# Kernel tuning notes

Measured on AMD Instinct MI355X. Metric: run time of the kernel, lower is better.

## Reference

```python
import jax, jax.numpy as jnp
import numpy as np

B, N, DIM, H, DH = 2, 2048, 512, 8, 64
EPS = 1e-3  # eps added after relu feature map, per original


def setup_inputs() -> dict:
    key = jax.random.key(0)
    k0, k1, k2, k3, k4 = jax.random.split(key, 5)
    s_in = 1.0 / np.sqrt(DIM)
    s_out = 1.0 / np.sqrt(H * DH)
    return {
        "x": jax.random.normal(k0, (B, N, DIM), jnp.float32),
        "Wq": jax.random.normal(k1, (DIM, H * DH), jnp.float32) * s_in,
        "Wk": jax.random.normal(k2, (DIM, H * DH), jnp.float32) * s_in,
        "Wv": jax.random.normal(k3, (DIM, H * DH), jnp.float32) * s_in,
        "Wo": jax.random.normal(k4, (H * DH, DIM), jnp.float32) * s_out,
        "bo": jnp.zeros((DIM,), jnp.float32),
    }


def causal_linear_attn(q, k, v, eps=EPS):
    # bucket_size == 1 path of the original causal_linear_attn (blindspot_size=1):
    # relu feature map + eps, running cumsums of k and of the outer product k v^T.
    q = jax.nn.relu(q) + eps
    k = jax.nn.relu(k) + eps
    k_cum = jnp.cumsum(k, axis=2)                                  # [b,h,n,d]
    ctx = jnp.cumsum(k[..., :, None] * v[..., None, :], axis=2)    # [b,h,n,d,e]
    d_inv = 1.0 / jnp.einsum('bhnd,bhnd->bhn', q, k_cum)           # [b,h,n]
    return jnp.einsum('bhnd,bhnde,bhn->bhne', q, ctx, d_inv)       # [b,h,n,e]


def reference(x, Wq, Wk, Wv, Wo, bo):
    b, n, _ = x.shape
    split = lambda t: t.reshape(b, n, H, DH).transpose(0, 2, 1, 3)  # [b,h,n,dh]
    q = split(x @ Wq)
    k = split(x @ Wk)
    v = split(x @ Wv)
    out = causal_linear_attn(q, k, v)
    out = out.transpose(0, 2, 1, 3).reshape(b, n, H * DH)
    return out @ Wo + bo
```

## Files before the change

### kernel.cpp

```cpp
#include <hip/hip_runtime.h>

constexpr int kB   = 2;
constexpr int kN   = 2048;
constexpr int kDIM = 512;
constexpr int kH   = 8;
constexpr int kDH  = 64;
constexpr int kBH  = kB * kH;
constexpr int NROWS = kB * kN;
constexpr int CHUNK = 64;
constexpr int NCH   = kN / CHUNK;
constexpr int CBSTRIDE = kDH * kDH + kDH;
constexpr float kEPS = 1e-3f;

typedef _Float16 f16x8 __attribute__((ext_vector_type(8)));
typedef _Float16 f16x4 __attribute__((ext_vector_type(4)));
typedef float    floatx4 __attribute__((ext_vector_type(4)));

__device__ __forceinline__ void async_copy16(void* lds, const void* g) {
    __builtin_amdgcn_global_load_lds(
        (const __attribute__((address_space(1))) void*)g,
        (__attribute__((address_space(3))) void*)lds,
        16, 0, 0);
}

__global__ __launch_bounds__(256)
void convert_x_kernel(const float* __restrict__ x, _Float16* __restrict__ xh)
{
    const int i = blockIdx.x * 256 + threadIdx.x;
    const float4 a = *(const float4*)(x + (size_t)i * 8);
    const float4 b = *(const float4*)(x + (size_t)i * 8 + 4);
    f16x8 o;
    o[0] = (_Float16)a.x; o[1] = (_Float16)a.y; o[2] = (_Float16)a.z; o[3] = (_Float16)a.w;
    o[4] = (_Float16)b.x; o[5] = (_Float16)b.y; o[6] = (_Float16)b.z; o[7] = (_Float16)b.w;
    *(f16x8*)(xh + (size_t)i * 8) = o;
}

__global__ __launch_bounds__(256)
void convert_wT_kernel(const float* __restrict__ Wq, const float* __restrict__ Wk,
                       const float* __restrict__ Wv, const float* __restrict__ Wo,
                       _Float16* __restrict__ WT, _Float16* __restrict__ WoT)
{
    __shared__ float tile[32][33];
    const int z = blockIdx.z;
    const float* src = (z == 0) ? Wq : (z == 1) ? Wk : (z == 2) ? Wv : Wo;
    _Float16* dst = (z < 3) ? (WT + (size_t)z * 512 * 512) : WoT;
    const int r0 = blockIdx.y * 32, c0 = blockIdx.x * 32;
    const int tr = threadIdx.x >> 5, tc = threadIdx.x & 31;
    #pragma unroll
    for (int i = 0; i < 4; ++i)
        tile[tr + 8 * i][tc] = src[(size_t)(r0 + tr + 8 * i) * 512 + c0 + tc];
    __syncthreads();
    #pragma unroll
    for (int i = 0; i < 4; ++i)
        dst[(size_t)(c0 + tr + 8 * i) * 512 + r0 + tc] = (_Float16)tile[tc][tr + 8 * i];
}

template<int MODE>
__global__ __launch_bounds__(256)
void mfma_gemm_kernel(const _Float16* __restrict__ A,
                      const _Float16* __restrict__ BT,
                      const float* __restrict__ bo,
                      float* __restrict__ outf,
                      _Float16* __restrict__ qh,
                      _Float16* __restrict__ khb,
                      _Float16* __restrict__ kTh,
                      _Float16* __restrict__ vTh)
{
    constexpr int BM = 128, BN = 128, BK = 64, K = 512;
    __shared__ _Float16 As[BM * BK];
    __shared__ _Float16 Bs[BN * BK];

    const int t = threadIdx.x;
    const int l = t & 63;
    const int w = t >> 6;
    const int wm = w >> 1, wn = w & 1;
    const int m0 = blockIdx.x * BM;
    const int n0 = blockIdx.y * BN;

    const int r15 = l & 15, kq = l >> 4, sw = r15 & 7;

    floatx4 acc[4][4];
    #pragma unroll
    for (int mi = 0; mi < 4; ++mi)
        #pragma unroll
        for (int ni = 0; ni < 4; ++ni)
            acc[mi][ni] = (floatx4){0.f, 0.f, 0.f, 0.f};

    const int srow  = t >> 3;
    const int sslot = t & 7;

    const char* Abase = (const char*)(A + (size_t)m0 * K);
    const char* Bbase = (const char*)(BT + (size_t)n0 * K);
    char* AsB = (char*)As;
    char* BsB = (char*)Bs;

    const char* ArdB = (const char*)As + (wm * 64 + r15) * 128;
    const char* BrdB = (const char*)Bs + (wn * 64 + r15) * 128;
    const int sw0 = ((kq ^ sw) << 4);
    const int sw1 = (((4 + kq) ^ sw) << 4);

    for (int k0 = 0; k0 < K; k0 += BK) {
        #pragma unroll
        for (int i = 0; i < 4; ++i) {
            const int row = i * 32 + srow;
            const int gsl = sslot ^ (row & 7);
            async_copy16(AsB + row * 128 + sslot * 16,
                         Abase + (size_t)row * (K * 2) + k0 * 2 + gsl * 16);
            async_copy16(BsB + row * 128 + sslot * 16,
                         Bbase + (size_t)row * (K * 2) + k0 * 2 + gsl * 16);
        }
        __syncthreads();

        f16x8 af[4][2], bf[4][2];
        #pragma unroll
        for (int i = 0; i < 4; ++i) {
            af[i][0] = *(const f16x8*)(ArdB + i * 2048 + sw0);
            af[i][1] = *(const f16x8*)(ArdB + i * 2048 + sw1);
            bf[i][0] = *(const f16x8*)(BrdB + i * 2048 + sw0);
            bf[i][1] = *(const f16x8*)(BrdB + i * 2048 + sw1);
        }
        #pragma unroll
        for (int kk = 0; kk < 2; ++kk)
            #pragma unroll
            for (int mi = 0; mi < 4; ++mi)
                #pragma unroll
                for (int ni = 0; ni < 4; ++ni)
                    acc[mi][ni] = __builtin_amdgcn_mfma_f32_16x16x32_f16(
                        af[mi][kk], bf[ni][kk], acc[mi][ni], 0, 0, 0);
        __syncthreads();
    }

    if (MODE == 0) {
        #pragma unroll
        for (int ni = 0; ni < 4; ++ni) {
            const int col = n0 + wn * 64 + ni * 16 + r15;
            const int which = col >> 9;
            const int h = (col >> 6) & 7, e = col & 63;
            #pragma unroll
            for (int mi = 0; mi < 4; ++mi) {
                const int row0 = m0 + wm * 64 + mi * 16 + kq * 4;
                const int b = row0 >> 11, nn = row0 & 2047;
                const int bh = b * 8 + h;
                float vv[4];
                #pragma unroll
                for (int r = 0; r < 4; ++r) {
                    float v = acc[mi][ni][r];
                    if (which < 2) v = fmaxf(v, 0.f) + kEPS;
                    vv[r] = v;
                }
                if (which == 0) {
                    #pragma unroll
                    for (int r = 0; r < 4; ++r)
                        qh[((size_t)bh * kN + nn + r) * 64 + e] = (_Float16)vv[r];
                } else if (which == 1) {
                    #pragma unroll
                    for (int r = 0; r < 4; ++r)
                        khb[((size_t)bh * kN + nn + r) * 64 + e] = (_Float16)vv[r];
                    f16x4 t4;
                    t4[0] = (_Float16)vv[0]; t4[1] = (_Float16)vv[1];
                    t4[2] = (_Float16)vv[2]; t4[3] = (_Float16)vv[3];
                    *(f16x4*)(kTh + ((size_t)bh * 64 + e) * kN + nn) = t4;
                } else {
                    f16x4 t4;
                    t4[0] = (_Float16)vv[0]; t4[1] = (_Float16)vv[1];
                    t4[2] = (_Float16)vv[2]; t4[3] = (_Float16)vv[3];
                    *(f16x4*)(vTh + ((size_t)bh * 64 + e) * kN + nn) = t4;
                }
            }
        }
    } else {
        #pragma unroll
        for (int ni = 0; ni < 4; ++ni) {
            const int col = n0 + wn * 64 + ni * 16 + r15;
            const float bias = bo[col];
            #pragma unroll
            for (int mi = 0; mi < 4; ++mi) {
                const int row = m0 + wm * 64 + mi * 16 + kq * 4;
                #pragma unroll
                for (int r = 0; r < 4; ++r)
                    outf[(size_t)(row + r) * 512 + col] = acc[mi][ni][r] + bias;
            }
        }
    }
}

__global__ __launch_bounds__(256)
void chunk_sum_kernel(const _Float16* __restrict__ kTh, const _Float16* __restrict__ vTh,
                      float* __restrict__ cbuf)
{
    const int ch = blockIdx.x, bh = blockIdx.y;
    const int t = threadIdx.x, l = t & 63, w = t >> 6;
    const int r15 = l & 15, kq = l >> 4;

    const _Float16* vbase = vTh + (size_t)bh * 64 * kN + ch * 64;
    const _Float16* kbase = kTh + (size_t)bh * 64 * kN + ch * 64;

    f16x8 av[2], bk[4][2];
    #pragma unroll
    for (int kk = 0; kk < 2; ++kk) {
        av[kk] = *(const f16x8*)(vbase + (size_t)(w * 16 + r15) * kN + kk * 32 + kq * 8);
        #pragma unroll
        for (int ni = 0; ni < 4; ++ni)
            bk[ni][kk] = *(const f16x8*)(kbase + (size_t)(ni * 16 + r15) * kN + kk * 32 + kq * 8);
    }
    floatx4 acc[4];
    #pragma unroll
    for (int ni = 0; ni < 4; ++ni) acc[ni] = (floatx4){0.f, 0.f, 0.f, 0.f};
    #pragma unroll
    for (int kk = 0; kk < 2; ++kk)
        #pragma unroll
        for (int ni = 0; ni < 4; ++ni)
            acc[ni] = __builtin_amdgcn_mfma_f32_16x16x32_f16(av[kk], bk[ni][kk], acc[ni], 0, 0, 0);

    float* out = cbuf + ((size_t)bh * NCH + ch) * CBSTRIDE;
    #pragma unroll
    for (int ni = 0; ni < 4; ++ni)
        #pragma unroll
        for (int r = 0; r < 4; ++r)
            out[(size_t)(w * 16 + kq * 4 + r) * 64 + ni * 16 + r15] = acc[ni][r];

    if (t < 64) {
        const _Float16* kp = kbase + (size_t)t * kN;
        float z = 0.f;
        #pragma unroll
        for (int j = 0; j < 8; ++j) {
            f16x8 v8 = *(const f16x8*)(kp + j * 8);
            #pragma unroll
            for (int u = 0; u < 8; ++u) z += (float)v8[u];
        }
        out[4096 + t] = z;
    }
}

__global__ __launch_bounds__(256)
void prefix_kernel(const float* __restrict__ cbuf, _Float16* __restrict__ spre16,
                   float* __restrict__ zpre)
{
    const int bh = blockIdx.y;
    const int i = blockIdx.x * 256 + threadIdx.x;
    if (i >= CBSTRIDE) return;
    const float* src = cbuf + (size_t)bh * NCH * CBSTRIDE + i;
    _Float16* dst = spre16 + (size_t)bh * NCH * CBSTRIDE + i;
    float* zp = zpre + (size_t)bh * NCH * 64;
    const bool isz = (i >= 4096);
    float vals[NCH];
    #pragma unroll
    for (int c = 0; c < NCH; ++c) vals[c] = src[(size_t)c * CBSTRIDE];
    float a = 0.f;
    #pragma unroll
    for (int c = 0; c < NCH; ++c) {
        dst[(size_t)c * CBSTRIDE] = (_Float16)a;
        if (isz) zp[c * 64 + (i - 4096)] = a;
        a += vals[c];
    }
}

__global__ __launch_bounds__(256)
void chunk_out_kernel(const _Float16* __restrict__ qh, const _Float16* __restrict__ khb,
                      const _Float16* __restrict__ vTh, const _Float16* __restrict__ spre16,
                      const float* __restrict__ zpre, _Float16* __restrict__ attnh)
{
    const int ch = blockIdx.x, bh = blockIdx.y;
    const int t = threadIdx.x, l = t & 63, w = t >> 6;
    const int r15 = l & 15, kq = l >> 4;

    __shared__ _Float16 Plds[64 * 64];
    __shared__ float denp[64];
    __shared__ float denf[64];

    const size_t rowbase = (size_t)bh * kN + ch * 64;

    f16x8 aq[2], bk[4][2];
    #pragma unroll
    for (int kk = 0; kk < 2; ++kk) {
        aq[kk] = *(const f16x8*)(qh + (rowbase + w * 16 + r15) * 64 + kk * 32 + kq * 8);
        #pragma unroll
        for (int ni = 0; ni < 4; ++ni)
            bk[ni][kk] = *(const f16x8*)(khb + (rowbase + ni * 16 + r15) * 64 + kk * 32 + kq * 8);
    }
    floatx4 sacc[4];
    #pragma unroll
    for (int ni = 0; ni < 4; ++ni) sacc[ni] = (floatx4){0.f, 0.f, 0.f, 0.f};
    #pragma unroll
    for (int kk = 0; kk < 2; ++kk)
        #pragma unroll
        for (int ni = 0; ni < 4; ++ni)
            sacc[ni] = __builtin_amdgcn_mfma_f32_16x16x32_f16(aq[kk], bk[ni][kk], sacc[ni], 0, 0, 0);

    const int qrow = w * 16 + kq * 4;
    float psum[4] = {0.f, 0.f, 0.f, 0.f};
    #pragma unroll
    for (int ni = 0; ni < 4; ++ni) {
        const int m = ni * 16 + r15;
        #pragma unroll
        for (int r = 0; r < 4; ++r) {
            const int row = qrow + r;
            const float v = (m <= row) ? sacc[ni][r] : 0.f;
            psum[r] += v;
            const int byte = row * 128 + ((((unsigned)m >> 3) ^ (row & 7)) << 4) + (m & 7) * 2;
            *(_Float16*)((char*)Plds + byte) = (_Float16)v;
        }
    }
    #pragma unroll
    for (int r = 0; r < 4; ++r) {
        float p = psum[r];
        p += __shfl_xor(p, 1, 16);
        p += __shfl_xor(p, 2, 16);
        p += __shfl_xor(p, 4, 16);
        p += __shfl_xor(p, 8, 16);
        if (r15 == 0) denp[qrow + r] = p;
    }
    __syncthreads();

    if (t < 64) {
        const _Float16* qp = qh + (rowbase + t) * 64;
        const float* zp = zpre + ((size_t)bh * NCH + ch) * 64;
        float s = denp[t];
        #pragma unroll
        for (int j = 0; j < 8; ++j) {
            f16x8 q8 = *(const f16x8*)(qp + j * 8);
            #pragma unroll
            for (int u = 0; u < 8; ++u) s += (float)q8[u] * zp[j * 8 + u];
        }
        denf[t] = 1.0f / s;
    }

    f16x8 ap[2], bv[4][2], bs[4][2];
    #pragma unroll
    for (int km = 0; km < 2; ++km)
        ap[km] = *(const f16x8*)((char*)Plds + (w * 16 + r15) * 128 +
                                 (((km * 4 + kq) ^ (r15 & 7)) << 4));
    #pragma unroll
    for (int ni = 0; ni < 4; ++ni) {
        #pragma unroll
        for (int km = 0; km < 2; ++km)
            bv[ni][km] = *(const f16x8*)(vTh + ((size_t)bh * 64 + ni * 16 + r15) * kN +
                                         ch * 64 + km * 32 + kq * 8);
    }
    const _Float16* sp = spre16 + ((size_t)bh * NCH + ch) * CBSTRIDE;
    #pragma unroll
    for (int ni = 0; ni < 4; ++ni)
        #pragma unroll
        for (int kd = 0; kd < 2; ++kd)
            bs[ni][kd] = *(const f16x8*)(sp + (size_t)(ni * 16 + r15) * 64 + kd * 32 + kq * 8);

    floatx4 oacc[4];
    #pragma unroll
    for (int ni = 0; ni < 4; ++ni) oacc[ni] = (floatx4){0.f, 0.f, 0.f, 0.f};
    #pragma unroll
    for (int km = 0; km < 2; ++km)
        #pragma unroll
        for (int ni = 0; ni < 4; ++ni)
            oacc[ni] = __builtin_amdgcn_mfma_f32_16x16x32_f16(ap[km], bv[ni][km], oacc[ni], 0, 0, 0);
    #pragma unroll
    for (int kd = 0; kd < 2; ++kd)
        #pragma unroll
        for (int ni = 0; ni < 4; ++ni)
            oacc[ni] = __builtin_amdgcn_mfma_f32_16x16x32_f16(aq[kd], bs[ni][kd], oacc[ni], 0, 0, 0);
    __syncthreads();

    const int b = bh >> 3, h = bh & 7;
    #pragma unroll
    for (int ni = 0; ni < 4; ++ni) {
        const int e = ni * 16 + r15;
        #pragma unroll
        for (int r = 0; r < 4; ++r) {
            const int qn = qrow + r;
            const float ov = oacc[ni][r] * denf[qn];
            attnh[((size_t)(b * kN + ch * 64 + qn)) * 512 + h * 64 + e] = (_Float16)ov;
        }
    }
}

extern "C" void kernel_launch(void* const* d_in, const int* in_sizes, int n_in,
                              void* d_out, int out_size, void* d_ws, size_t ws_size,
                              hipStream_t stream)
{
    const float* x  = (const float*)d_in[0];
    const float* Wq = (const float*)d_in[1];
    const float* Wk = (const float*)d_in[2];
    const float* Wv = (const float*)d_in[3];
    const float* Wo = (const float*)d_in[4];
    const float* bo = (const float*)d_in[5];
    float* out = (float*)d_out;

    char* ws = (char*)d_ws;
    _Float16* qh     = (_Float16*)(ws + 0);
    _Float16* khb    = (_Float16*)(ws + 4194304);
    _Float16* kTh    = (_Float16*)(ws + 8388608);
    _Float16* vTh    = (_Float16*)(ws + 12582912);
    float*    cbuf   = (float*)(ws + 16777216);
    _Float16* spre16 = (_Float16*)(ws + 25296896);
    float*    zpre   = (float*)(ws + 29556736);
    _Float16* xh     = (_Float16*)(ws + 29687808);
    _Float16* WT     = (_Float16*)(ws + 33882112);
    _Float16* WoT    = (_Float16*)(ws + 35454976);
    _Float16* attnh  = xh;

    convert_x_kernel<<<1024, 256, 0, stream>>>(x, xh);
    convert_wT_kernel<<<dim3(16, 16, 4), 256, 0, stream>>>(Wq, Wk, Wv, Wo, WT, WoT);
    mfma_gemm_kernel<0><<<dim3(NROWS / 128, 12), 256, 0, stream>>>(
        xh, WT, nullptr, nullptr, qh, khb, kTh, vTh);
    chunk_sum_kernel<<<dim3(NCH, kBH), 256, 0, stream>>>(kTh, vTh, cbuf);
    prefix_kernel<<<dim3(17, kBH), 256, 0, stream>>>(cbuf, spre16, zpre);
    chunk_out_kernel<<<dim3(NCH, kBH), 256, 0, stream>>>(qh, khb, vTh, spre16, zpre, attnh);
    mfma_gemm_kernel<1><<<dim3(NROWS / 128, 4), 256, 0, stream>>>(
        attnh, WoT, bo, out, nullptr, nullptr, nullptr, nullptr);
}
```

Baseline: 56.48 us.

## Fuse attention stages with grid barriers and convert x inside QKV GEMM

Merges the chunk-sum, prefix-scan and chunk-output kernels into one persistent kernel that synchronises the whole grid with atomic-counter barriers. The fp32-to-fp16 conversion of x moves into the QKV GEMM's A-tile load, which removes the separate convert kernel and its round trip through memory. The grid is transposed so consecutive blocks share an A row tile. This cuts four launches in exchange for spin-wait barriers, which deadlock unless all 512 blocks are co-resident, and it replaces the async A loads with synchronous converting loads.

```diff
diff --git a/kernel.cpp b/kernel.cpp
--- a/kernel.cpp
+++ b/kernel.cpp
@@ -23,23 +23,26 @@
         16, 0, 0);
 }
 
+__device__ __forceinline__ void grid_barrier(unsigned* cnt, unsigned target) {
+    __syncthreads();
+    if (threadIdx.x == 0) {
+        __threadfence();
+        __hip_atomic_fetch_add(cnt, 1u, __ATOMIC_ACQ_REL, __HIP_MEMORY_SCOPE_AGENT);
+        while (__hip_atomic_load(cnt, __ATOMIC_ACQUIRE, __HIP_MEMORY_SCOPE_AGENT) < target)
+            __builtin_amdgcn_s_sleep(2);
+        __threadfence();
+    }
+    __syncthreads();
+}
+
 __global__ __launch_bounds__(256)
-void convert_x_kernel(const float* __restrict__ x, _Float16* __restrict__ xh)
+void prep_kernel(const float* __restrict__ Wq, const float* __restrict__ Wk,
+                 const float* __restrict__ Wv, const float* __restrict__ Wo,
+                 _Float16* __restrict__ WT, _Float16* __restrict__ WoT,
+                 unsigned* __restrict__ cnt)
 {
-    const int i = blockIdx.x * 256 + threadIdx.x;
-    const float4 a = *(const float4*)(x + (size_t)i * 8);
-    const float4 b = *(const float4*)(x + (size_t)i * 8 + 4);
-    f16x8 o;
-    o[0] = (_Float16)a.x; o[1] = (_Float16)a.y; o[2] = (_Float16)a.z; o[3] = (_Float16)a.w;
-    o[4] = (_Float16)b.x; o[5] = (_Float16)b.y; o[6] = (_Float16)b.z; o[7] = (_Float16)b.w;
-    *(f16x8*)(xh + (size_t)i * 8) = o;
-}
-
-__global__ __launch_bounds__(256)
-void convert_wT_kernel(const float* __restrict__ Wq, const float* __restrict__ Wk,
-                       const float* __restrict__ Wv, const float* __restrict__ Wo,
-                       _Float16* __restrict__ WT, _Float16* __restrict__ WoT)
-{
+    if (blockIdx.x == 0 && blockIdx.y == 0 && blockIdx.z == 0 && threadIdx.x < 4)
+        cnt[threadIdx.x] = 0u;
     __shared__ float tile[32][33];
     const int z = blockIdx.z;
     const float* src = (z == 0) ? Wq : (z == 1) ? Wk : (z == 2) ? Wv : Wo;
@@ -57,7 +60,8 @@
 
 template<int MODE>
 __global__ __launch_bounds__(256)
-void mfma_gemm_kernel(const _Float16* __restrict__ A,
+void mfma_gemm_kernel(const float* __restrict__ Af32,
+                      const _Float16* __restrict__ Af16,
                       const _Float16* __restrict__ BT,
                       const float* __restrict__ bo,
                       float* __restrict__ outf,
@@ -66,16 +70,16 @@
                       _Float16* __restrict__ kTh,
                       _Float16* __restrict__ vTh)
 {
-    constexpr int BM = 128, BN = 128, BK = 64, K = 512;
-    __shared__ _Float16 As[BM * BK];
-    __shared__ _Float16 Bs[BN * BK];
+    constexpr int K = 512;
+    __shared__ _Float16 As[128 * 64];
+    __shared__ _Float16 Bs[128 * 64];
 
     const int t = threadIdx.x;
     const int l = t & 63;
     const int w = t >> 6;
     const int wm = w >> 1, wn = w & 1;
-    const int m0 = blockIdx.x * BM;
-    const int n0 = blockIdx.y * BN;
+    const int m0 = blockIdx.y * 128;
+    const int n0 = blockIdx.x * 128;
 
     const int r15 = l & 15, kq = l >> 4, sw = r15 & 7;
 
@@ -89,7 +93,6 @@
     const int srow  = t >> 3;
     const int sslot = t & 7;
 
-    const char* Abase = (const char*)(A + (size_t)m0 * K);
     const char* Bbase = (const char*)(BT + (size_t)n0 * K);
     char* AsB = (char*)As;
     char* BsB = (char*)Bs;
@@ -99,15 +102,38 @@
     const int sw0 = ((kq ^ sw) << 4);
     const int sw1 = (((4 + kq) ^ sw) << 4);
 
-    for (int k0 = 0; k0 < K; k0 += BK) {
+    for (int k0 = 0; k0 < K; k0 += 64) {
         #pragma unroll
         for (int i = 0; i < 4; ++i) {
             const int row = i * 32 + srow;
             const int gsl = sslot ^ (row & 7);
-            async_copy16(AsB + row * 128 + sslot * 16,
-                         Abase + (size_t)row * (K * 2) + k0 * 2 + gsl * 16);
             async_copy16(BsB + row * 128 + sslot * 16,
                          Bbase + (size_t)row * (K * 2) + k0 * 2 + gsl * 16);
+        }
+        if (MODE == 0) {
+            #pragma unroll
+            for (int i = 0; i < 4; ++i) {
+                const int s = i * 256 + t;
+                const int row = s >> 3, sl = s & 7;
+                const float* xp = Af32 + (size_t)(m0 + row) * K + k0 + sl * 8;
+                const float4 a0 = *(const float4*)(xp);
+                const float4 a1 = *(const float4*)(xp + 4);
+                f16x8 v;
+                v[0] = (_Float16)a0.x; v[1] = (_Float16)a0.y;
+                v[2] = (_Float16)a0.z; v[3] = (_Float16)a0.w;
+                v[4] = (_Float16)a1.x; v[5] = (_Float16)a1.y;
+                v[6] = (_Float16)a1.z; v[7] = (_Float16)a1.w;
+                *(f16x8*)(AsB + row * 128 + ((sl ^ (row & 7)) << 4)) = v;
+            }
+        } else {
+            const char* Abase = (const char*)(Af16 + (size_t)m0 * K);
+            #pragma unroll
+            for (int i = 0; i < 4; ++i) {
+                const int row = i * 32 + srow;
+                const int gsl = sslot ^ (row & 7);
+                async_copy16(AsB + row * 128 + sslot * 16,
+                             Abase + (size_t)row * (K * 2) + k0 * 2 + gsl * 16);
+            }
         }
         __syncthreads();
 
@@ -185,88 +211,87 @@
 }
 
 __global__ __launch_bounds__(256)
-void chunk_sum_kernel(const _Float16* __restrict__ kTh, const _Float16* __restrict__ vTh,
-                      float* __restrict__ cbuf)
+void mid_kernel(const _Float16* __restrict__ qh, const _Float16* __restrict__ khb,
+                const _Float16* __restrict__ kTh, const _Float16* __restrict__ vTh,
+                float* __restrict__ cbuf, _Float16* __restrict__ spre16,
+                float* __restrict__ zpre, _Float16* __restrict__ attnh,
+                unsigned* __restrict__ cnt)
 {
     const int ch = blockIdx.x, bh = blockIdx.y;
     const int t = threadIdx.x, l = t & 63, w = t >> 6;
     const int r15 = l & 15, kq = l >> 4;
 
-    const _Float16* vbase = vTh + (size_t)bh * 64 * kN + ch * 64;
-    const _Float16* kbase = kTh + (size_t)bh * 64 * kN + ch * 64;
-
-    f16x8 av[2], bk[4][2];
-    #pragma unroll
-    for (int kk = 0; kk < 2; ++kk) {
-        av[kk] = *(const f16x8*)(vbase + (size_t)(w * 16 + r15) * kN + kk * 32 + kq * 8);
-        #pragma unroll
-        for (int ni = 0; ni < 4; ++ni)
-            bk[ni][kk] = *(const f16x8*)(kbase + (size_t)(ni * 16 + r15) * kN + kk * 32 + kq * 8);
-    }
-    floatx4 acc[4];
-    #pragma unroll
-    for (int ni = 0; ni < 4; ++ni) acc[ni] = (floatx4){0.f, 0.f, 0.f, 0.f};
-    #pragma unroll
-    for (int kk = 0; kk < 2; ++kk)
-        #pragma unroll
-        for (int ni = 0; ni < 4; ++ni)
-            acc[ni] = __builtin_amdgcn_mfma_f32_16x16x32_f16(av[kk], bk[ni][kk], acc[ni], 0, 0, 0);
-
-    float* out = cbuf + ((size_t)bh * NCH + ch) * CBSTRIDE;
-    #pragma unroll
-    for (int ni = 0; ni < 4; ++ni)
-        #pragma unroll
-        for (int r = 0; r < 4; ++r)
-            out[(size_t)(w * 16 + kq * 4 + r) * 64 + ni * 16 + r15] = acc[ni][r];
-
-    if (t < 64) {
-        const _Float16* kp = kbase + (size_t)t * kN;
-        float z = 0.f;
-        #pragma unroll
-        for (int j = 0; j < 8; ++j) {
-            f16x8 v8 = *(const f16x8*)(kp + j * 8);
-            #pragma unroll
-            for (int u = 0; u < 8; ++u) z += (float)v8[u];
-        }
-        out[4096 + t] = z;
-    }
-}
-
-__global__ __launch_bounds__(256)
-void prefix_kernel(const float* __restrict__ cbuf, _Float16* __restrict__ spre16,
-                   float* __restrict__ zpre)
-{
-    const int bh = blockIdx.y;
-    const int i = blockIdx.x * 256 + threadIdx.x;
-    if (i >= CBSTRIDE) return;
-    const float* src = cbuf + (size_t)bh * NCH * CBSTRIDE + i;
-    _Float16* dst = spre16 + (size_t)bh * NCH * CBSTRIDE + i;
-    float* zp = zpre + (size_t)bh * NCH * 64;
-    const bool isz = (i >= 4096);
-    float vals[NCH];
-    #pragma unroll
-    for (int c = 0; c < NCH; ++c) vals[c] = src[(size_t)c * CBSTRIDE];
-    float a = 0.f;
-    #pragma unroll
-    for (int c = 0; c < NCH; ++c) {
-        dst[(size_t)c * CBSTRIDE] = (_Float16)a;
-        if (isz) zp[c * 64 + (i - 4096)] = a;
-        a += vals[c];
-    }
-}
-
-__global__ __launch_bounds__(256)
-void chunk_out_kernel(const _Float16* __restrict__ qh, const _Float16* __restrict__ khb,
-                      const _Float16* __restrict__ vTh, const _Float16* __restrict__ spre16,
-                      const float* __restrict__ zpre, _Float16* __restrict__ attnh)
-{
-    const int ch = blockIdx.x, bh = blockIdx.y;
-    const int t = threadIdx.x, l = t & 63, w = t >> 6;
-    const int r15 = l & 15, kq = l >> 4;
-
     __shared__ _Float16 Plds[64 * 64];
     __shared__ float denp[64];
     __shared__ float denf[64];
+
+    {
+        const _Float16* vbase = vTh + (size_t)bh * 64 * kN + ch * 64;
+        const _Float16* kbase = kTh + (size_t)bh * 64 * kN + ch * 64;
+        f16x8 av[2], bk[4][2];
+        #pragma unroll
+        for (int kk = 0; kk < 2; ++kk) {
+            av[kk] = *(const f16x8*)(vbase + (size_t)(w * 16 + r15) * kN + kk * 32 + kq * 8);
+            #pragma unroll
+            for (int ni = 0; ni < 4; ++ni)
+                bk[ni][kk] = *(const f16x8*)(kbase + (size_t)(ni * 16 + r15) * kN + kk * 32 + kq * 8);
+        }
+        floatx4 sa[4];
+        #pragma unroll
+        for (int ni = 0; ni < 4; ++ni) sa[ni] = (floatx4){0.f, 0.f, 0.f, 0.f};
+        #pragma unroll
+        for (int kk = 0; kk < 2; ++kk)
+            #pragma unroll
+            for (int ni = 0; ni < 4; ++ni)
+                sa[ni] = __builtin_amdgcn_mfma_f32_16x16x32_f16(av[kk], bk[ni][kk], sa[ni], 0, 0, 0);
+
+        float* outp = cbuf + ((size_t)bh * NCH + ch) * CBSTRIDE;
+        #pragma unroll
+        for (int ni = 0; ni < 4; ++ni)
+            #pragma unroll
+            for (int r = 0; r < 4; ++r)
+                outp[(size_t)(w * 16 + kq * 4 + r) * 64 + ni * 16 + r15] = sa[ni][r];
+
+        if (t < 64) {
+            const _Float16* kp = kbase + (size_t)t * kN;
+            float z = 0.f;
+            #pragma unroll
+            for (int j = 0; j < 8; ++j) {
+                f16x8 v8 = *(const f16x8*)(kp + j * 8);
+                #pragma unroll
+                for (int u = 0; u < 8; ++u) z += (float)v8[u];
+            }
+            outp[4096 + t] = z;
+        }
+    }
+    grid_barrier(cnt, NCH * kBH);
+
+    {
+        const int col = ch * 130 + t;
+        if (t < 130) {
+            const float* src = cbuf + (size_t)bh * NCH * CBSTRIDE + col;
+            float vals[NCH];
+            #pragma unroll
+            for (int c = 0; c < NCH; ++c) vals[c] = src[(size_t)c * CBSTRIDE];
+            float a = 0.f;
+            if (col < 4096) {
+                _Float16* dst = spre16 + (size_t)bh * NCH * CBSTRIDE + col;
+                #pragma unroll
+                for (int c = 0; c < NCH; ++c) {
+                    dst[(size_t)c * CBSTRIDE] = (_Float16)a;
+                    a += vals[c];
+                }
+            } else {
+                float* zp = zpre + (size_t)bh * NCH * 64 + (col - 4096);
+                #pragma unroll
+                for (int c = 0; c < NCH; ++c) {
+                    zp[c * 64] = a;
+                    a += vals[c];
+                }
+            }
+        }
+    }
+    grid_barrier(cnt, 2 * NCH * kBH);
 
     const size_t rowbase = (size_t)bh * kN + ch * 64;
 
@@ -392,18 +417,16 @@
     float*    cbuf   = (float*)(ws + 16777216);
     _Float16* spre16 = (_Float16*)(ws + 25296896);
     float*    zpre   = (float*)(ws + 29556736);
-    _Float16* xh     = (_Float16*)(ws + 29687808);
+    _Float16* attnh  = (_Float16*)(ws + 29687808);
     _Float16* WT     = (_Float16*)(ws + 33882112);
     _Float16* WoT    = (_Float16*)(ws + 35454976);
-    _Float16* attnh  = xh;
-
-    convert_x_kernel<<<1024, 256, 0, stream>>>(x, xh);
-    convert_wT_kernel<<<dim3(16, 16, 4), 256, 0, stream>>>(Wq, Wk, Wv, Wo, WT, WoT);
-    mfma_gemm_kernel<0><<<dim3(NROWS / 128, 12), 256, 0, stream>>>(
-        xh, WT, nullptr, nullptr, qh, khb, kTh, vTh);
-    chunk_sum_kernel<<<dim3(NCH, kBH), 256, 0, stream>>>(kTh, vTh, cbuf);
-    prefix_kernel<<<dim3(17, kBH), 256, 0, stream>>>(cbuf, spre16, zpre);
-    chunk_out_kernel<<<dim3(NCH, kBH), 256, 0, stream>>>(qh, khb, vTh, spre16, zpre, attnh);
-    mfma_gemm_kernel<1><<<dim3(NROWS / 128, 4), 256, 0, stream>>>(
-        attnh, WoT, bo, out, nullptr, nullptr, nullptr, nullptr);
-}
+    unsigned* cnt    = (unsigned*)(ws + 35979264);
+
+    prep_kernel<<<dim3(16, 16, 4), 256, 0, stream>>>(Wq, Wk, Wv, Wo, WT, WoT, cnt);
+    mfma_gemm_kernel<0><<<dim3(12, NROWS / 128), 256, 0, stream>>>(
+        x, nullptr, WT, nullptr, nullptr, qh, khb, kTh, vTh);
+    mid_kernel<<<dim3(NCH, kBH), 256, 0, stream>>>(
+        qh, khb, kTh, vTh, cbuf, spre16, zpre, attnh, cnt);
+    mfma_gemm_kernel<1><<<dim3(4, NROWS / 128), 256, 0, stream>>>(
+        nullptr, attnh, WoT, bo, out, nullptr, nullptr, nullptr, nullptr);
+}
```

Measured after the change: 175.9 us. +211.5%, slower.

## Fuse x conversion into QKV GEMM and fuse output projection into chunk kernel

Applied to the files above, without the earlier changes.

The QKV GEMM now loads fp32 x directly and converts it to fp16 while staging into LDS, which removes the separate convert kernel and its round trip through global memory. The chunk output kernel becomes a 512-thread block that covers all 8 heads of a 64-row chunk. It stages the normalized attention output in LDS and immediately runs the Wo projection plus bias, writing the final fp32 output. This removes two launches and the attnh buffer traffic. The cost is fewer, larger blocks (64 in the epilogue) with WoT fragments read straight from global memory, and the A operand in the QKV GEMM is now loaded synchronously.

```diff
diff --git a/kernel.cpp b/kernel.cpp
--- a/kernel.cpp
+++ b/kernel.cpp
@@ -24,21 +24,9 @@
 }
 
 __global__ __launch_bounds__(256)
-void convert_x_kernel(const float* __restrict__ x, _Float16* __restrict__ xh)
-{
-    const int i = blockIdx.x * 256 + threadIdx.x;
-    const float4 a = *(const float4*)(x + (size_t)i * 8);
-    const float4 b = *(const float4*)(x + (size_t)i * 8 + 4);
-    f16x8 o;
-    o[0] = (_Float16)a.x; o[1] = (_Float16)a.y; o[2] = (_Float16)a.z; o[3] = (_Float16)a.w;
-    o[4] = (_Float16)b.x; o[5] = (_Float16)b.y; o[6] = (_Float16)b.z; o[7] = (_Float16)b.w;
-    *(f16x8*)(xh + (size_t)i * 8) = o;
-}
-
-__global__ __launch_bounds__(256)
-void convert_wT_kernel(const float* __restrict__ Wq, const float* __restrict__ Wk,
-                       const float* __restrict__ Wv, const float* __restrict__ Wo,
-                       _Float16* __restrict__ WT, _Float16* __restrict__ WoT)
+void prep_kernel(const float* __restrict__ Wq, const float* __restrict__ Wk,
+                 const float* __restrict__ Wv, const float* __restrict__ Wo,
+                 _Float16* __restrict__ WT, _Float16* __restrict__ WoT)
 {
     __shared__ float tile[32][33];
     const int z = blockIdx.z;
@@ -55,27 +43,24 @@
         dst[(size_t)(c0 + tr + 8 * i) * 512 + r0 + tc] = (_Float16)tile[tc][tr + 8 * i];
 }
 
-template<int MODE>
 __global__ __launch_bounds__(256)
-void mfma_gemm_kernel(const _Float16* __restrict__ A,
-                      const _Float16* __restrict__ BT,
-                      const float* __restrict__ bo,
-                      float* __restrict__ outf,
-                      _Float16* __restrict__ qh,
-                      _Float16* __restrict__ khb,
-                      _Float16* __restrict__ kTh,
-                      _Float16* __restrict__ vTh)
-{
-    constexpr int BM = 128, BN = 128, BK = 64, K = 512;
-    __shared__ _Float16 As[BM * BK];
-    __shared__ _Float16 Bs[BN * BK];
+void qkv_gemm_kernel(const float* __restrict__ Af32,
+                     const _Float16* __restrict__ BT,
+                     _Float16* __restrict__ qh,
+                     _Float16* __restrict__ khb,
+                     _Float16* __restrict__ kTh,
+                     _Float16* __restrict__ vTh)
+{
+    constexpr int K = 512;
+    __shared__ _Float16 As[128 * 64];
+    __shared__ _Float16 Bs[128 * 64];
 
     const int t = threadIdx.x;
     const int l = t & 63;
     const int w = t >> 6;
     const int wm = w >> 1, wn = w & 1;
-    const int m0 = blockIdx.x * BM;
-    const int n0 = blockIdx.y * BN;
+    const int m0 = blockIdx.y * 128;
+    const int n0 = blockIdx.x * 128;
 
     const int r15 = l & 15, kq = l >> 4, sw = r15 & 7;
 
@@ -89,7 +74,6 @@
     const int srow  = t >> 3;
     const int sslot = t & 7;
 
-    const char* Abase = (const char*)(A + (size_t)m0 * K);
     const char* Bbase = (const char*)(BT + (size_t)n0 * K);
     char* AsB = (char*)As;
     char* BsB = (char*)Bs;
@@ -99,15 +83,27 @@
     const int sw0 = ((kq ^ sw) << 4);
     const int sw1 = (((4 + kq) ^ sw) << 4);
 
-    for (int k0 = 0; k0 < K; k0 += BK) {
+    for (int k0 = 0; k0 < K; k0 += 64) {
         #pragma unroll
         for (int i = 0; i < 4; ++i) {
             const int row = i * 32 + srow;
             const int gsl = sslot ^ (row & 7);
-            async_copy16(AsB + row * 128 + sslot * 16,
-                         Abase + (size_t)row * (K * 2) + k0 * 2 + gsl * 16);
             async_copy16(BsB + row * 128 + sslot * 16,
                          Bbase + (size_t)row * (K * 2) + k0 * 2 + gsl * 16);
+        }
+        #pragma unroll
+        for (int i = 0; i < 4; ++i) {
+            const int s = i * 256 + t;
+            const int row = s >> 3, sl = s & 7;
+            const float* xp = Af32 + (size_t)(m0 + row) * K + k0 + sl * 8;
+            const float4 a0 = *(const float4*)(xp);
+            const float4 a1 = *(const float4*)(xp + 4);
+            f16x8 v;
+            v[0] = (_Float16)a0.x; v[1] = (_Float16)a0.y;
+            v[2] = (_Float16)a0.z; v[3] = (_Float16)a0.w;
+            v[4] = (_Float16)a1.x; v[5] = (_Float16)a1.y;
+            v[6] = (_Float16)a1.z; v[7] = (_Float16)a1.w;
+            *(f16x8*)(AsB + row * 128 + ((sl ^ (row & 7)) << 4)) = v;
         }
         __syncthreads();
 
@@ -130,55 +126,40 @@
         __syncthreads();
     }
 
-    if (MODE == 0) {
-        #pragma unroll
-        for (int ni = 0; ni < 4; ++ni) {
-            const int col = n0 + wn * 64 + ni * 16 + r15;
-            const int which = col >> 9;
-            const int h = (col >> 6) & 7, e = col & 63;
-            #pragma unroll
-            for (int mi = 0; mi < 4; ++mi) {
-                const int row0 = m0 + wm * 64 + mi * 16 + kq * 4;
-                const int b = row0 >> 11, nn = row0 & 2047;
-                const int bh = b * 8 + h;
-                float vv[4];
-                #pragma unroll
-                for (int r = 0; r < 4; ++r) {
-                    float v = acc[mi][ni][r];
-                    if (which < 2) v = fmaxf(v, 0.f) + kEPS;
-                    vv[r] = v;
-                }
-                if (which == 0) {
-                    #pragma unroll
-                    for (int r = 0; r < 4; ++r)
-                        qh[((size_t)bh * kN + nn + r) * 64 + e] = (_Float16)vv[r];
-                } else if (which == 1) {
-                    #pragma unroll
-                    for (int r = 0; r < 4; ++r)
-                        khb[((size_t)bh * kN + nn + r) * 64 + e] = (_Float16)vv[r];
-                    f16x4 t4;
-                    t4[0] = (_Float16)vv[0]; t4[1] = (_Float16)vv[1];
-                    t4[2] = (_Float16)vv[2]; t4[3] = (_Float16)vv[3];
-                    *(f16x4*)(kTh + ((size_t)bh * 64 + e) * kN + nn) = t4;
-                } else {
-                    f16x4 t4;
-                    t4[0] = (_Float16)vv[0]; t4[1] = (_Float16)vv[1];
-                    t4[2] = (_Float16)vv[2]; t4[3] = (_Float16)vv[3];
-                    *(f16x4*)(vTh + ((size_t)bh * 64 + e) * kN + nn) = t4;
-                }
+    #pragma unroll
+    for (int ni = 0; ni < 4; ++ni) {
+        const int col = n0 + wn * 64 + ni * 16 + r15;
+        const int which = col >> 9;
+        const int h = (col >> 6) & 7, e = col & 63;
+        #pragma unroll
+        for (int mi = 0; mi < 4; ++mi) {
+            const int row0 = m0 + wm * 64 + mi * 16 + kq * 4;
+            const int b = row0 >> 11, nn = row0 & 2047;
+            const int bh = b * 8 + h;
+            float vv[4];
+            #pragma unroll
+            for (int r = 0; r < 4; ++r) {
+                float v = acc[mi][ni][r];
+                if (which < 2) v = fmaxf(v, 0.f) + kEPS;
+                vv[r] = v;
             }
-        }
-    } else {
-        #pragma unroll
-        for (int ni = 0; ni < 4; ++ni) {
-            const int col = n0 + wn * 64 + ni * 16 + r15;
-            const float bias = bo[col];
-            #pragma unroll
-            for (int mi = 0; mi < 4; ++mi) {
-                const int row = m0 + wm * 64 + mi * 16 + kq * 4;
+            if (which == 0) {
                 #pragma unroll
                 for (int r = 0; r < 4; ++r)
-                    outf[(size_t)(row + r) * 512 + col] = acc[mi][ni][r] + bias;
+                    qh[((size_t)bh * kN + nn + r) * 64 + e] = (_Float16)vv[r];
+            } else if (which == 1) {
+                #pragma unroll
+                for (int r = 0; r < 4; ++r)
+                    khb[((size_t)bh * kN + nn + r) * 64 + e] = (_Float16)vv[r];
+                f16x4 t4;
+                t4[0] = (_Float16)vv[0]; t4[1] = (_Float16)vv[1];
+                t4[2] = (_Float16)vv[2]; t4[3] = (_Float16)vv[3];
+                *(f16x4*)(kTh + ((size_t)bh * 64 + e) * kN + nn) = t4;
+            } else {
+                f16x4 t4;
+                t4[0] = (_Float16)vv[0]; t4[1] = (_Float16)vv[1];
+                t4[2] = (_Float16)vv[2]; t4[3] = (_Float16)vv[3];
+                *(f16x4*)(vTh + ((size_t)bh * 64 + e) * kN + nn) = t4;
             }
         }
     }
@@ -255,88 +236,121 @@
     }
 }
 
-__global__ __launch_bounds__(256)
-void chunk_out_kernel(const _Float16* __restrict__ qh, const _Float16* __restrict__ khb,
-                      const _Float16* __restrict__ vTh, const _Float16* __restrict__ spre16,
-                      const float* __restrict__ zpre, _Float16* __restrict__ attnh)
-{
-    const int ch = blockIdx.x, bh = blockIdx.y;
-    const int t = threadIdx.x, l = t & 63, w = t >> 6;
+__global__ __launch_bounds__(512, 2)
+void chunk_epilogue_kernel(const _Float16* __restrict__ qh,
+                           const _Float16* __restrict__ khb,
+                           const _Float16* __restrict__ vTh,
+                           const _Float16* __restrict__ spre16,
+                           const float* __restrict__ zpre,
+                           const _Float16* __restrict__ WoT,
+                           const float* __restrict__ bo,
+                           float* __restrict__ outf)
+{
+    const int ch = blockIdx.x;
+    const int b  = blockIdx.y;
+    const int t = threadIdx.x;
+    const int w = t >> 6;
+    const int l = t & 63;
     const int r15 = l & 15, kq = l >> 4;
-
-    __shared__ _Float16 Plds[64 * 64];
-    __shared__ float denp[64];
-    __shared__ float denf[64];
-
-    const size_t rowbase = (size_t)bh * kN + ch * 64;
-
-    f16x8 aq[2], bk[4][2];
-    #pragma unroll
-    for (int kk = 0; kk < 2; ++kk) {
-        aq[kk] = *(const f16x8*)(qh + (rowbase + w * 16 + r15) * 64 + kk * 32 + kq * 8);
-        #pragma unroll
-        for (int ni = 0; ni < 4; ++ni)
-            bk[ni][kk] = *(const f16x8*)(khb + (rowbase + ni * 16 + r15) * 64 + kk * 32 + kq * 8);
-    }
-    floatx4 sacc[4];
-    #pragma unroll
-    for (int ni = 0; ni < 4; ++ni) sacc[ni] = (floatx4){0.f, 0.f, 0.f, 0.f};
-    #pragma unroll
-    for (int kk = 0; kk < 2; ++kk)
-        #pragma unroll
-        for (int ni = 0; ni < 4; ++ni)
-            sacc[ni] = __builtin_amdgcn_mfma_f32_16x16x32_f16(aq[kk], bk[ni][kk], sacc[ni], 0, 0, 0);
-
-    const int qrow = w * 16 + kq * 4;
-    float psum[4] = {0.f, 0.f, 0.f, 0.f};
-    #pragma unroll
-    for (int ni = 0; ni < 4; ++ni) {
-        const int m = ni * 16 + r15;
+    const int h = w;
+    const int bh = b * 8 + h;
+
+    __shared__ char smem[65536];
+    __shared__ float denp[8][64];
+    __shared__ float denf[8][64];
+
+    const size_t rowbase = (size_t)bh * kN + (size_t)ch * 64;
+
+    f16x8 aq[4][2];
+    #pragma unroll
+    for (int mi = 0; mi < 4; ++mi)
+        #pragma unroll
+        for (int kk = 0; kk < 2; ++kk)
+            aq[mi][kk] = *(const f16x8*)(qh + (rowbase + mi * 16 + r15) * 64 + kk * 32 + kq * 8);
+
+    floatx4 sacc[4][4];
+    #pragma unroll
+    for (int mi = 0; mi < 4; ++mi)
+        #pragma unroll
+        for (int ni = 0; ni < 4; ++ni)
+            sacc[mi][ni] = (floatx4){0.f, 0.f, 0.f, 0.f};
+    {
+        f16x8 bk[4][2];
+        #pragma unroll
+        for (int ni = 0; ni < 4; ++ni)
+            #pragma unroll
+            for (int kk = 0; kk < 2; ++kk)
+                bk[ni][kk] = *(const f16x8*)(khb + (rowbase + ni * 16 + r15) * 64 + kk * 32 + kq * 8);
+        #pragma unroll
+        for (int kk = 0; kk < 2; ++kk)
+            #pragma unroll
+            for (int mi = 0; mi < 4; ++mi)
+                #pragma unroll
+                for (int ni = 0; ni < 4; ++ni)
+                    sacc[mi][ni] = __builtin_amdgcn_mfma_f32_16x16x32_f16(
+                        aq[mi][kk], bk[ni][kk], sacc[mi][ni], 0, 0, 0);
+    }
+
+    char* P = smem + h * 8192;
+    float psum[4][4];
+    #pragma unroll
+    for (int mi = 0; mi < 4; ++mi)
+        #pragma unroll
+        for (int r = 0; r < 4; ++r) psum[mi][r] = 0.f;
+    #pragma unroll
+    for (int mi = 0; mi < 4; ++mi) {
+        #pragma unroll
+        for (int ni = 0; ni < 4; ++ni) {
+            const int m = ni * 16 + r15;
+            #pragma unroll
+            for (int r = 0; r < 4; ++r) {
+                const int row = mi * 16 + kq * 4 + r;
+                const float v = (m <= row) ? sacc[mi][ni][r] : 0.f;
+                psum[mi][r] += v;
+                const int byte = row * 128 + ((((unsigned)m >> 3) ^ (row & 7)) << 4) + (m & 7) * 2;
+                *(_Float16*)(P + byte) = (_Float16)v;
+            }
+        }
+    }
+    #pragma unroll
+    for (int mi = 0; mi < 4; ++mi) {
         #pragma unroll
         for (int r = 0; r < 4; ++r) {
-            const int row = qrow + r;
-            const float v = (m <= row) ? sacc[ni][r] : 0.f;
-            psum[r] += v;
-            const int byte = row * 128 + ((((unsigned)m >> 3) ^ (row & 7)) << 4) + (m & 7) * 2;
-            *(_Float16*)((char*)Plds + byte) = (_Float16)v;
-        }
-    }
-    #pragma unroll
-    for (int r = 0; r < 4; ++r) {
-        float p = psum[r];
-        p += __shfl_xor(p, 1, 16);
-        p += __shfl_xor(p, 2, 16);
-        p += __shfl_xor(p, 4, 16);
-        p += __shfl_xor(p, 8, 16);
-        if (r15 == 0) denp[qrow + r] = p;
-    }
-    __syncthreads();
-
-    if (t < 64) {
-        const _Float16* qp = qh + (rowbase + t) * 64;
+            float p = psum[mi][r];
+            p += __shfl_xor(p, 1, 16);
+            p += __shfl_xor(p, 2, 16);
+            p += __shfl_xor(p, 4, 16);
+            p += __shfl_xor(p, 8, 16);
+            if (r15 == 0) denp[h][mi * 16 + kq * 4 + r] = p;
+        }
+    }
+
+    {
+        const _Float16* qp = qh + (rowbase + l) * 64;
         const float* zp = zpre + ((size_t)bh * NCH + ch) * 64;
-        float s = denp[t];
+        float s = denp[h][l];
         #pragma unroll
         for (int j = 0; j < 8; ++j) {
             f16x8 q8 = *(const f16x8*)(qp + j * 8);
             #pragma unroll
             for (int u = 0; u < 8; ++u) s += (float)q8[u] * zp[j * 8 + u];
         }
-        denf[t] = 1.0f / s;
-    }
-
-    f16x8 ap[2], bv[4][2], bs[4][2];
-    #pragma unroll
-    for (int km = 0; km < 2; ++km)
-        ap[km] = *(const f16x8*)((char*)Plds + (w * 16 + r15) * 128 +
-                                 (((km * 4 + kq) ^ (r15 & 7)) << 4));
-    #pragma unroll
-    for (int ni = 0; ni < 4; ++ni) {
+        denf[h][l] = 1.0f / s;
+    }
+
+    f16x8 ap[4][2], bv[4][2], bs[4][2];
+    #pragma unroll
+    for (int mi = 0; mi < 4; ++mi)
+        #pragma unroll
+        for (int km = 0; km < 2; ++km)
+            ap[mi][km] = *(const f16x8*)(P + (mi * 16 + r15) * 128 +
+                                         (((km * 4 + kq) ^ (r15 & 7)) << 4));
+    #pragma unroll
+    for (int ni = 0; ni < 4; ++ni)
         #pragma unroll
         for (int km = 0; km < 2; ++km)
             bv[ni][km] = *(const f16x8*)(vTh + ((size_t)bh * 64 + ni * 16 + r15) * kN +
                                          ch * 64 + km * 32 + kq * 8);
-    }
     const _Float16* sp = spre16 + ((size_t)bh * NCH + ch) * CBSTRIDE;
     #pragma unroll
     for (int ni = 0; ni < 4; ++ni)
@@ -344,30 +358,85 @@
         for (int kd = 0; kd < 2; ++kd)
             bs[ni][kd] = *(const f16x8*)(sp + (size_t)(ni * 16 + r15) * 64 + kd * 32 + kq * 8);
 
-    floatx4 oacc[4];
-    #pragma unroll
-    for (int ni = 0; ni < 4; ++ni) oacc[ni] = (floatx4){0.f, 0.f, 0.f, 0.f};
+    floatx4 oacc[4][4];
+    #pragma unroll
+    for (int mi = 0; mi < 4; ++mi)
+        #pragma unroll
+        for (int ni = 0; ni < 4; ++ni)
+            oacc[mi][ni] = (floatx4){0.f, 0.f, 0.f, 0.f};
     #pragma unroll
     for (int km = 0; km < 2; ++km)
         #pragma unroll
-        for (int ni = 0; ni < 4; ++ni)
-            oacc[ni] = __builtin_amdgcn_mfma_f32_16x16x32_f16(ap[km], bv[ni][km], oacc[ni], 0, 0, 0);
+        for (int mi = 0; mi < 4; ++mi)
+            #pragma unroll
+            for (int ni = 0; ni < 4; ++ni)
+                oacc[mi][ni] = __builtin_amdgcn_mfma_f32_16x16x32_f16(
+                    ap[mi][km], bv[ni][km], oacc[mi][ni], 0, 0, 0);
     #pragma unroll
     for (int kd = 0; kd < 2; ++kd)
         #pragma unroll
-        for (int ni = 0; ni < 4; ++ni)
-            oacc[ni] = __builtin_amdgcn_mfma_f32_16x16x32_f16(aq[kd], bs[ni][kd], oacc[ni], 0, 0, 0);
+        for (int mi = 0; mi < 4; ++mi)
+            #pragma unroll
+            for (int ni = 0; ni < 4; ++ni)
+                oacc[mi][ni] = __builtin_amdgcn_mfma_f32_16x16x32_f16(
+                    aq[mi][kd], bs[ni][kd], oacc[mi][ni], 0, 0, 0);
+
     __syncthreads();
 
-    const int b = bh >> 3, h = bh & 7;
+    #pragma unroll
+    for (int mi = 0; mi < 4; ++mi) {
+        #pragma unroll
+        for (int ni = 0; ni < 4; ++ni) {
+            const int c = h * 64 + ni * 16 + r15;
+            const int slot = c >> 3;
+            #pragma unroll
+            for (int r = 0; r < 4; ++r) {
+                const int row = mi * 16 + kq * 4 + r;
+                const float ov = oacc[mi][ni][r] * denf[h][row];
+                const int byte = row * 1024 + ((slot ^ (row & 7)) << 4) + (c & 7) * 2;
+                *(_Float16*)(smem + byte) = (_Float16)ov;
+            }
+        }
+    }
+    __syncthreads();
+
+    floatx4 acc2[4][4];
+    #pragma unroll
+    for (int mi = 0; mi < 4; ++mi)
+        #pragma unroll
+        for (int ni = 0; ni < 4; ++ni)
+            acc2[mi][ni] = (floatx4){0.f, 0.f, 0.f, 0.f};
+
+    for (int kk = 0; kk < 16; ++kk) {
+        f16x8 af2[4], bf2[4];
+        #pragma unroll
+        for (int mi = 0; mi < 4; ++mi) {
+            const int row = mi * 16 + r15;
+            af2[mi] = *(const f16x8*)(smem + row * 1024 + (((kk * 4 + kq) ^ (row & 7)) << 4));
+        }
+        #pragma unroll
+        for (int ni = 0; ni < 4; ++ni)
+            bf2[ni] = *(const f16x8*)(WoT + ((size_t)(w * 64 + ni * 16 + r15)) * 512 +
+                                      kk * 32 + kq * 8);
+        #pragma unroll
+        for (int mi = 0; mi < 4; ++mi)
+            #pragma unroll
+            for (int ni = 0; ni < 4; ++ni)
+                acc2[mi][ni] = __builtin_amdgcn_mfma_f32_16x16x32_f16(
+                    af2[mi], bf2[ni], acc2[mi][ni], 0, 0, 0);
+    }
+
     #pragma unroll
     for (int ni = 0; ni < 4; ++ni) {
-        const int e = ni * 16 + r15;
-        #pragma unroll
-        for (int r = 0; r < 4; ++r) {
-            const int qn = qrow + r;
-            const float ov = oacc[ni][r] * denf[qn];
-            attnh[((size_t)(b * kN + ch * 64 + qn)) * 512 + h * 64 + e] = (_Float16)ov;
+        const int col = w * 64 + ni * 16 + r15;
+        const float bias = bo[col];
+        #pragma unroll
+        for (int mi = 0; mi < 4; ++mi) {
+            #pragma unroll
+            for (int r = 0; r < 4; ++r) {
+                const int rowg = b * 2048 + ch * 64 + mi * 16 + kq * 4 + r;
+                outf[(size_t)rowg * 512 + col] = acc2[mi][ni][r] + bias;
+            }
         }
     }
 }
@@ -392,18 +461,14 @@
     float*    cbuf   = (float*)(ws + 16777216);
     _Float16* spre16 = (_Float16*)(ws + 25296896);
     float*    zpre   = (float*)(ws + 29556736);
-    _Float16* xh     = (_Float16*)(ws + 29687808);
-    _Float16* WT     = (_Float16*)(ws + 33882112);
-    _Float16* WoT    = (_Float16*)(ws + 35454976);
-    _Float16* attnh  = xh;
-
-    convert_x_kernel<<<1024, 256, 0, stream>>>(x, xh);
-    convert_wT_kernel<<<dim3(16, 16, 4), 256, 0, stream>>>(Wq, Wk, Wv, Wo, WT, WoT);
-    mfma_gemm_kernel<0><<<dim3(NROWS / 128, 12), 256, 0, stream>>>(
-        xh, WT, nullptr, nullptr, qh, khb, kTh, vTh);
+    _Float16* WT     = (_Float16*)(ws + 29687808);
+    _Float16* WoT    = (_Float16*)(ws + 31260672);
+
+    prep_kernel<<<dim3(16, 16, 4), 256, 0, stream>>>(Wq, Wk, Wv, Wo, WT, WoT);
+    qkv_gemm_kernel<<<dim3(12, NROWS / 128), 256, 0, stream>>>(
+        x, WT, qh, khb, kTh, vTh);
     chunk_sum_kernel<<<dim3(NCH, kBH), 256, 0, stream>>>(kTh, vTh, cbuf);
     prefix_kernel<<<dim3(17, kBH), 256, 0, stream>>>(cbuf, spre16, zpre);
-    chunk_out_kernel<<<dim3(NCH, kBH), 256, 0, stream>>>(qh, khb, vTh, spre16, zpre, attnh);
-    mfma_gemm_kernel<1><<<dim3(NROWS / 128, 4), 256, 0, stream>>>(
-        attnh, WoT, bo, out, nullptr, nullptr, nullptr, nullptr);
-}
+    chunk_epilogue_kernel<<<dim3(NCH, kB), 512, 0, stream>>>(
+        qh, khb, vTh, spre16, zpre, WoT, bo, out);
+}
```

Result: slower. 72.85 us (+29.0%).
